# Performance work log

Measured on AMD Instinct MI355X. Metric: run time of the kernel, lower is better.

Reference implementation:

```python
import jax, jax.numpy as jnp
import numpy as np

N_HEAD = 16
N_EMBD = 64  # per-head dim in this module's convention
INNER = N_HEAD * N_EMBD  # 1024


def setup_inputs() -> dict:
    key = jax.random.key(0)
    ks = jax.random.split(key, 6)
    B, S = 4, 2048
    scale = 0.02
    return {
        "x": jax.random.normal(ks[0], (B, S, N_EMBD), dtype=jnp.float32),
        "Wq": jax.random.normal(ks[1], (N_EMBD, INNER), dtype=jnp.float32) * scale,
        "Wk": jax.random.normal(ks[2], (N_EMBD, INNER), dtype=jnp.float32) * scale,
        "Wv": jax.random.normal(ks[3], (N_EMBD, INNER), dtype=jnp.float32) * scale,
        "Wo": jax.random.normal(ks[4], (INNER, N_EMBD), dtype=jnp.float32) * scale,
        "bo": jax.random.normal(ks[5], (N_EMBD,), dtype=jnp.float32) * scale,
        "causal_mask": 1,
    }


def reference(x, Wq, Wk, Wv, Wo, bo, causal_mask):
    B, S, _ = x.shape
    # projections: [B,S,INNER] -> [B,H,S,D]
    def split_heads(t):
        return t.reshape(B, S, N_HEAD, N_EMBD).transpose(0, 2, 1, 3)
    q = split_heads(x @ Wq)
    k = split_heads(x @ Wk)
    v = split_heads(x @ Wv)
    # [B,H,S,S]
    scores = jnp.einsum("bhqd,bhkd->bhqk", q, k) / jnp.sqrt(jnp.float32(N_EMBD))
    if causal_mask:
        future = jnp.triu(jnp.ones((S, S), dtype=scores.dtype), k=1)
        scores = scores - 1e9 * future  # matches torch: subtract 1e9*mask
    attn = jax.nn.softmax(scores, axis=-1)
    out = jnp.einsum("bhqk,bhkd->bhqd", attn, v)
    out = out.transpose(0, 2, 1, 3).reshape(B, S, INNER)
    return out @ Wo + bo
```

## Files before the change

kernel.cpp:

```cpp
#include <hip/hip_runtime.h>
#include <hip/hip_bf16.h>

#define NHEAD 16
#define HDIM 64
#define DINNER 1024
#define NBATCH 4
#define SEQ 2048
#define NTOK (NBATCH*SEQ)

typedef __bf16 bf16;
typedef __bf16 bf16x4 __attribute__((ext_vector_type(4)));
typedef __bf16 bf16x8 __attribute__((ext_vector_type(8)));
typedef float f32x4 __attribute__((ext_vector_type(4)));

#define OFF_BO   8
#define OFF_XB   128
#define OFF_WQT  (OFF_XB + NTOK*HDIM)
#define OFF_WKT  (OFF_WQT + DINNER*HDIM)
#define OFF_WVT  (OFF_WKT + DINNER*HDIM)
#define OFF_WOT  (OFF_WVT + DINNER*HDIM)
#define OFF_Q    (OFF_WOT + DINNER*HDIM)
#define OFF_K    (OFF_Q + NTOK*DINNER)
#define OFF_VT   (OFF_K + NTOK*DINNER)
#define OFF_ATT  (OFF_VT + NTOK*DINNER)

#define SSCALE 0.18033688011112042f

static __device__ __forceinline__ bf16x8 ld8(const bf16* p) {
  return *reinterpret_cast<const bf16x8*>(p);
}

static __device__ __forceinline__ int detect_isbf(const void* x, int tid,
                                                  int* sflag) {
  if (tid < 64) {
    const unsigned short* xb = (const unsigned short*)x;
    bool ok = true;
#pragma unroll
    for (int i = 0; i < 8; i++) {
      unsigned e = (xb[tid * 8 + i] >> 7) & 0xFF;
      ok = ok && (e >= 64 && e <= 140);
    }
    unsigned long long mball = __ballot(ok);
    if (tid == 0) *sflag = (mball == ~0ull) ? 1 : 0;
  }
  __syncthreads();
  return *sflag;
}

__global__ __launch_bounds__(256) void prep_kernel(
    const void* __restrict__ x, const void* __restrict__ Wq,
    const void* __restrict__ Wk, const void* __restrict__ Wv,
    const void* __restrict__ Wo, const void* __restrict__ bo,
    bf16* __restrict__ ws) {
  __shared__ int sflag;
  int isbf = detect_isbf(x, threadIdx.x, &sflag);
  int z = blockIdx.y;
  int idx = blockIdx.x * 256 + threadIdx.x;
  if (z < 3) {
    const void* src = (z == 0) ? Wq : (z == 1) ? Wk : Wv;
    bf16* dst = ws + ((z == 0) ? OFF_WQT : (z == 1) ? OFF_WKT : OFF_WVT);
    int d = idx >> 10, n = idx & 1023;
    float v = isbf ? (float)((const bf16*)src)[idx] : ((const float*)src)[idx];
    if (z == 0) v *= SSCALE;
    dst[n * HDIM + d] = (bf16)v;
  } else if (z == 3) {
    int k = idx >> 6, n = idx & 63;
    float v = isbf ? (float)((const bf16*)Wo)[idx] : ((const float*)Wo)[idx];
    ws[OFF_WOT + n * DINNER + k] = (bf16)v;
  } else if (z == 4) {
    int i = idx * 8;
    bf16x8 v;
    if (isbf) {
      v = ld8((const bf16*)x + i);
    } else {
      f32x4 a = *reinterpret_cast<const f32x4*>((const float*)x + i);
      f32x4 b2 = *reinterpret_cast<const f32x4*>((const float*)x + i + 4);
#pragma unroll
      for (int j = 0; j < 4; j++) { v[j] = (bf16)a[j]; v[4 + j] = (bf16)b2[j]; }
    }
    *reinterpret_cast<bf16x8*>(&ws[OFF_XB + i]) = v;
  } else {
    if (idx < 64) ws[OFF_BO + idx] = isbf ? ((const bf16*)bo)[idx] : (bf16)((const float*)bo)[idx];
  }
}

__global__ __launch_bounds__(256) void qkv_kernel(bf16* __restrict__ ws) {
  __shared__ __align__(16) bf16 Vst[4][16 * 72];
  int tt = blockIdx.x, pz = blockIdx.z;
  int w = threadIdx.x >> 6;
  int nc = blockIdx.y * 4 + w;
  int lane = threadIdx.x & 63;
  int lq = lane & 15, quad = lane >> 4;
  const bf16* WT = ws + OFF_WQT + pz * (DINNER * HDIM);
  int n0 = nc * 64;
  bf16x8 w0[4], w1[4];
#pragma unroll
  for (int c = 0; c < 4; c++) {
    const bf16* wr = WT + (n0 + c * 16 + lq) * HDIM;
    w0[c] = ld8(wr + quad * 8);
    w1[c] = ld8(wr + 32 + quad * 8);
  }
  bf16* Qb = ws + OFF_Q;
  bf16* Kb = ws + OFF_K;
  bf16* VTb = ws + OFF_VT;
  bf16x8 ao0[4], ao1[4];
  if (pz == 2) {
    const bf16* WoT = ws + OFF_WOT;
#pragma unroll
    for (int c = 0; c < 4; c++) {
      const bf16* orow = WoT + (size_t)(c * 16 + lq) * DINNER + nc * 64;
      ao0[c] = ld8(orow + quad * 8);
      ao1[c] = ld8(orow + 32 + quad * 8);
    }
  }
#pragma unroll
  for (int mi = 0; mi < 4; mi++) {
    int t0 = tt * 64 + mi * 16;
    const bf16* xrow = ws + OFF_XB + (t0 + lq) * HDIM;
    bf16x8 x0 = ld8(xrow + quad * 8);
    bf16x8 x1 = ld8(xrow + 32 + quad * 8);
    int b = t0 >> 11, s0 = t0 & (SEQ - 1);
    if (pz < 2) {
#pragma unroll
      for (int c = 0; c < 4; c++) {
        f32x4 z = {0.f, 0.f, 0.f, 0.f};
        z = __builtin_amdgcn_mfma_f32_16x16x32_bf16(w0[c], x0, z, 0, 0, 0);
        z = __builtin_amdgcn_mfma_f32_16x16x32_bf16(w1[c], x1, z, 0, 0, 0);
        bf16x4 pk = {(bf16)z[0], (bf16)z[1], (bf16)z[2], (bf16)z[3]};
        bf16* P = (pz == 0) ? Qb : Kb;
        *reinterpret_cast<bf16x4*>(
            &P[((size_t)(b * NHEAD + nc) * SEQ + s0 + lq) * HDIM + c * 16 + quad * 4]) = pk;
      }
    } else {
#pragma unroll
      for (int c = 0; c < 4; c++) {
        f32x4 z = {0.f, 0.f, 0.f, 0.f};
        z = __builtin_amdgcn_mfma_f32_16x16x32_bf16(w0[c], x0, z, 0, 0, 0);
        z = __builtin_amdgcn_mfma_f32_16x16x32_bf16(w1[c], x1, z, 0, 0, 0);
        bf16x4 pk = {(bf16)z[0], (bf16)z[1], (bf16)z[2], (bf16)z[3]};
        *reinterpret_cast<bf16x4*>(&Vst[w][lq * 72 + c * 16 + quad * 4]) = pk;
      }
      bf16x8 bv0 = ld8(&Vst[w][lq * 72 + quad * 8]);
      bf16x8 bv1 = ld8(&Vst[w][lq * 72 + 32 + quad * 8]);
#pragma unroll
      for (int c = 0; c < 4; c++) {
        f32x4 z2 = {0.f, 0.f, 0.f, 0.f};
        z2 = __builtin_amdgcn_mfma_f32_16x16x32_bf16(ao0[c], bv0, z2, 0, 0, 0);
        z2 = __builtin_amdgcn_mfma_f32_16x16x32_bf16(ao1[c], bv1, z2, 0, 0, 0);
#pragma unroll
        for (int r = 0; r < 4; r++) {
          int d = c * 16 + quad * 4 + r;
          VTb[(((size_t)b * NHEAD + nc) * HDIM + d) * SEQ + s0 + lq] = (bf16)z2[r];
        }
      }
    }
  }
}

__global__ __launch_bounds__(256, 2) void flash_kernel(const int* __restrict__ cmask,
                                                       bf16* __restrict__ ws) {
  __shared__ __align__(16) bf16 Kl[2][64 * 64];
  __shared__ __align__(16) bf16 Vl[2][64 * 64];
  __shared__ __align__(16) bf16 Pl[4][16 * 64];
  const int qmap[16] = {15,13,11,9,0,2,4,6,14,12,10,8,1,3,5,7};
  int bid = blockIdx.x;
  int bh = (bid & 7) * 8 + ((bid >> 3) & 7);
  int qt = qmap[bid >> 6];
  int w = threadIdx.x >> 6;
  int lane = threadIdx.x & 63;
  int lq = lane & 15, quad = lane >> 4;
  int causal = cmask[0];
  const bf16* Q = ws + OFF_Q + (size_t)bh * SEQ * HDIM;
  const bf16* K = ws + OFF_K + (size_t)bh * SEQ * HDIM;
  const bf16* VT = ws + OFF_VT + (size_t)bh * HDIM * SEQ;
  int b = bh >> 4, h = bh & 15;
  bf16* ar = ws + OFF_ATT;
  int sr = threadIdx.x >> 2;
  int sg = (threadIdx.x & 3) * 16;
  int sc0 = (((threadIdx.x & 3) * 2) ^ (sr & 7)) << 3;
  int sc1 = (((threadIdx.x & 3) * 2 + 1) ^ (sr & 7)) << 3;
  int rq0 = (quad ^ (lq & 7)) << 3;
  int rq1 = ((4 + quad) ^ (lq & 7)) << 3;

  int qb = qt * 128;
  int qw = qb + w * 32;
  int T = (causal ? (qb + 128) : SEQ) / 64;

  bf16x8 bq[2][2];
#pragma unroll
  for (int m = 0; m < 2; m++) {
    const bf16* qrow = Q + (qw + m * 16 + lq) * HDIM;
    bq[m][0] = ld8(qrow + quad * 8);
    bq[m][1] = ld8(qrow + 32 + quad * 8);
  }
  f32x4 o[2][4];
  float lsum[2] = {0.f, 0.f};
#pragma unroll
  for (int m = 0; m < 2; m++)
#pragma unroll
    for (int c = 0; c < 4; c++) o[m][c] = (f32x4){0.f, 0.f, 0.f, 0.f};

  bf16x8 kst0 = ld8(K + sr * HDIM + sg);
  bf16x8 kst1 = ld8(K + sr * HDIM + sg + 8);
  bf16x8 vst0 = ld8(VT + sr * SEQ + sg);
  bf16x8 vst1 = ld8(VT + sr * SEQ + sg + 8);

  for (int ti = 0; ti < T; ti++) {
    int buf = ti & 1;
    int k0 = ti * 64;
    *reinterpret_cast<bf16x8*>(&Kl[buf][sr * 64 + sc0]) = kst0;
    *reinterpret_cast<bf16x8*>(&Kl[buf][sr * 64 + sc1]) = kst1;
    *reinterpret_cast<bf16x8*>(&Vl[buf][sr * 64 + sc0]) = vst0;
    *reinterpret_cast<bf16x8*>(&Vl[buf][sr * 64 + sc1]) = vst1;
    int kn = (ti + 1 < T) ? (k0 + 64) : k0;
    kst0 = ld8(K + (kn + sr) * HDIM + sg);
    kst1 = ld8(K + (kn + sr) * HDIM + sg + 8);
    vst0 = ld8(VT + sr * SEQ + kn + sg);
    vst1 = ld8(VT + sr * SEQ + kn + sg + 8);
    __syncthreads();
    f32x4 st[2][4];
#pragma unroll
    for (int t = 0; t < 4; t++) {
      bf16x8 a0 = ld8(&Kl[buf][(t * 16 + lq) * 64 + rq0]);
      bf16x8 a1 = ld8(&Kl[buf][(t * 16 + lq) * 64 + rq1]);
#pragma unroll
      for (int m = 0; m < 2; m++) {
        f32x4 z = {0.f, 0.f, 0.f, 0.f};
        z = __builtin_amdgcn_mfma_f32_16x16x32_bf16(a0, bq[m][0], z, 0, 0, 0);
        z = __builtin_amdgcn_mfma_f32_16x16x32_bf16(a1, bq[m][1], z, 0, 0, 0);
        st[m][t] = z;
      }
    }
    bool needmask = causal && (k0 + 63 > qw);
    bf16x8 bp[2][2];
#pragma unroll
    for (int m = 0; m < 2; m++) {
      if (needmask) {
        int qrel = qw + m * 16 + lq - k0 - quad * 4;
#pragma unroll
        for (int t = 0; t < 4; t++)
#pragma unroll
          for (int r = 0; r < 4; r++)
            if (t * 16 + r > qrel) st[m][t][r] = -200.0f;
      }
      float sum = 0.f;
#pragma unroll
      for (int t = 0; t < 4; t++) {
        float e0 = exp2f(st[m][t][0]);
        float e1 = exp2f(st[m][t][1]);
        float e2 = exp2f(st[m][t][2]);
        float e3 = exp2f(st[m][t][3]);
        sum += (e0 + e1) + (e2 + e3);
        bf16x4 pk = {(bf16)e0, (bf16)e1, (bf16)e2, (bf16)e3};
        int ch = ((t * 2 + (quad >> 1)) ^ (lq & 7)) << 3;
        *reinterpret_cast<bf16x4*>(&Pl[w][lq * 64 + ch + (quad & 1) * 4]) = pk;
      }
      lsum[m] += sum;
      bp[m][0] = ld8(&Pl[w][lq * 64 + rq0]);
      bp[m][1] = ld8(&Pl[w][lq * 64 + rq1]);
    }
#pragma unroll
    for (int c = 0; c < 4; c++) {
      bf16x8 av0 = ld8(&Vl[buf][(c * 16 + lq) * 64 + rq0]);
      bf16x8 av1 = ld8(&Vl[buf][(c * 16 + lq) * 64 + rq1]);
#pragma unroll
      for (int m = 0; m < 2; m++) {
        o[m][c] = __builtin_amdgcn_mfma_f32_16x16x32_bf16(av0, bp[m][0], o[m][c], 0, 0, 0);
        o[m][c] = __builtin_amdgcn_mfma_f32_16x16x32_bf16(av1, bp[m][1], o[m][c], 0, 0, 0);
      }
    }
  }
#pragma unroll
  for (int m = 0; m < 2; m++) {
    lsum[m] += __shfl_xor(lsum[m], 16);
    lsum[m] += __shfl_xor(lsum[m], 32);
    float inv = 1.0f / lsum[m];
    size_t rowoff = ((size_t)(b * SEQ + qw + m * 16 + lq)) * DINNER + h * HDIM;
#pragma unroll
    for (int c = 0; c < 4; c++) {
      bf16x4 ov = {(bf16)(o[m][c][0] * inv), (bf16)(o[m][c][1] * inv),
                   (bf16)(o[m][c][2] * inv), (bf16)(o[m][c][3] * inv)};
      *reinterpret_cast<bf16x4*>(&ar[rowoff + c * 16 + quad * 4]) = ov;
    }
  }
}

__global__ __launch_bounds__(256) void reduce_kernel(const bf16* __restrict__ ws,
                                                     const void* __restrict__ x,
                                                     void* __restrict__ outp) {
  __shared__ int sflag;
  int isbf = detect_isbf(x, threadIdx.x, &sflag);
  int idx = blockIdx.x * 256 + threadIdx.x;
  int t = idx >> 6, d = idx & 63;
  const bf16* ar = ws + OFF_ATT + (size_t)t * DINNER + d;
  float s = (float)ws[OFF_BO + d];
#pragma unroll
  for (int h = 0; h < 16; h++) s += (float)ar[h * 64];
  if (isbf) ((bf16*)outp)[idx] = (bf16)s;
  else      ((float*)outp)[idx] = s;
}

extern "C" void kernel_launch(void* const* d_in, const int* in_sizes, int n_in,
                              void* d_out, int out_size, void* d_ws, size_t ws_size,
                              hipStream_t stream) {
  const void* x  = d_in[0];
  const void* Wq = d_in[1];
  const void* Wk = d_in[2];
  const void* Wv = d_in[3];
  const void* Wo = d_in[4];
  const void* bo = d_in[5];
  const int* cm  = (const int*)d_in[6];
  bf16* ws = (bf16*)d_ws;

  hipLaunchKernelGGL(prep_kernel, dim3(256, 6), dim3(256), 0, stream,
                     x, Wq, Wk, Wv, Wo, bo, ws);
  hipLaunchKernelGGL(qkv_kernel, dim3(128, 4, 3), dim3(256), 0, stream, ws);
  hipLaunchKernelGGL(flash_kernel, dim3(1024), dim3(256), 0, stream, cm, ws);
  hipLaunchKernelGGL(reduce_kernel, dim3(2048), dim3(256), 0, stream, ws, x, d_out);
}
```

Before: 161.8 us.

## Split causal KV range across paired query tiles for balanced flash blocks

Each flash block now handles a complementary pair of query tiles (z and 15-z) and processes one half of their combined KV tile range. This gives every block an equal amount of causal work. Unnormalized partial outputs and row sums are written to two workspace copies, and the reduce kernel merges them and normalizes. The launch-bounds occupancy hint is raised to 4. The split doubles the attention-output write and read traffic, and storing unnormalized accumulators in bf16 may cost some precision.

```diff
diff --git a/kernel.cpp b/kernel.cpp
--- a/kernel.cpp
+++ b/kernel.cpp
@@ -23,6 +23,8 @@
 #define OFF_K    (OFF_Q + NTOK*DINNER)
 #define OFF_VT   (OFF_K + NTOK*DINNER)
 #define OFF_ATT  (OFF_VT + NTOK*DINNER)
+#define OFF_ATT2 (OFF_ATT + NTOK*DINNER)
+#define OFF_L    (OFF_ATT2 + NTOK*DINNER)
 
 #define SSCALE 0.18033688011112042f
 
@@ -157,15 +159,15 @@
   }
 }
 
-__global__ __launch_bounds__(256, 2) void flash_kernel(const int* __restrict__ cmask,
+__global__ __launch_bounds__(256, 4) void flash_kernel(const int* __restrict__ cmask,
                                                        bf16* __restrict__ ws) {
   __shared__ __align__(16) bf16 Kl[2][64 * 64];
   __shared__ __align__(16) bf16 Vl[2][64 * 64];
   __shared__ __align__(16) bf16 Pl[4][16 * 64];
-  const int qmap[16] = {15,13,11,9,0,2,4,6,14,12,10,8,1,3,5,7};
   int bid = blockIdx.x;
   int bh = (bid & 7) * 8 + ((bid >> 3) & 7);
-  int qt = qmap[bid >> 6];
+  int z = (bid >> 6) & 7;
+  int half = bid >> 9;
   int w = threadIdx.x >> 6;
   int lane = threadIdx.x & 63;
   int lq = lane & 15, quad = lane >> 4;
@@ -174,7 +176,8 @@
   const bf16* K = ws + OFF_K + (size_t)bh * SEQ * HDIM;
   const bf16* VT = ws + OFF_VT + (size_t)bh * HDIM * SEQ;
   int b = bh >> 4, h = bh & 15;
-  bf16* ar = ws + OFF_ATT;
+  bf16* ar = ws + OFF_ATT + (size_t)half * NTOK * DINNER;
+  float* Lp = reinterpret_cast<float*>(ws + OFF_L) + (size_t)half * NTOK * NHEAD;
   int sr = threadIdx.x >> 2;
   int sg = (threadIdx.x & 3) * 16;
   int sc0 = (((threadIdx.x & 3) * 2) ^ (sr & 7)) << 3;
@@ -182,105 +185,120 @@
   int rq0 = (quad ^ (lq & 7)) << 3;
   int rq1 = ((4 + quad) ^ (lq & 7)) << 3;
 
-  int qb = qt * 128;
-  int qw = qb + w * 32;
-  int T = (causal ? (qb + 128) : SEQ) / 64;
-
-  bf16x8 bq[2][2];
-#pragma unroll
-  for (int m = 0; m < 2; m++) {
-    const bf16* qrow = Q + (qw + m * 16 + lq) * HDIM;
-    bq[m][0] = ld8(qrow + quad * 8);
-    bq[m][1] = ld8(qrow + 32 + quad * 8);
-  }
-  f32x4 o[2][4];
-  float lsum[2] = {0.f, 0.f};
-#pragma unroll
-  for (int m = 0; m < 2; m++)
-#pragma unroll
-    for (int c = 0; c < 4; c++) o[m][c] = (f32x4){0.f, 0.f, 0.f, 0.f};
-
-  bf16x8 kst0 = ld8(K + sr * HDIM + sg);
-  bf16x8 kst1 = ld8(K + sr * HDIM + sg + 8);
-  bf16x8 vst0 = ld8(VT + sr * SEQ + sg);
-  bf16x8 vst1 = ld8(VT + sr * SEQ + sg + 8);
-
-  for (int ti = 0; ti < T; ti++) {
-    int buf = ti & 1;
-    int k0 = ti * 64;
-    *reinterpret_cast<bf16x8*>(&Kl[buf][sr * 64 + sc0]) = kst0;
-    *reinterpret_cast<bf16x8*>(&Kl[buf][sr * 64 + sc1]) = kst1;
-    *reinterpret_cast<bf16x8*>(&Vl[buf][sr * 64 + sc0]) = vst0;
-    *reinterpret_cast<bf16x8*>(&Vl[buf][sr * 64 + sc1]) = vst1;
-    int kn = (ti + 1 < T) ? (k0 + 64) : k0;
-    kst0 = ld8(K + (kn + sr) * HDIM + sg);
-    kst1 = ld8(K + (kn + sr) * HDIM + sg + 8);
-    vst0 = ld8(VT + sr * SEQ + kn + sg);
-    vst1 = ld8(VT + sr * SEQ + kn + sg + 8);
-    __syncthreads();
-    f32x4 st[2][4];
-#pragma unroll
-    for (int t = 0; t < 4; t++) {
-      bf16x8 a0 = ld8(&Kl[buf][(t * 16 + lq) * 64 + rq0]);
-      bf16x8 a1 = ld8(&Kl[buf][(t * 16 + lq) * 64 + rq1]);
-#pragma unroll
-      for (int m = 0; m < 2; m++) {
-        f32x4 z = {0.f, 0.f, 0.f, 0.f};
-        z = __builtin_amdgcn_mfma_f32_16x16x32_bf16(a0, bq[m][0], z, 0, 0, 0);
-        z = __builtin_amdgcn_mfma_f32_16x16x32_bf16(a1, bq[m][1], z, 0, 0, 0);
-        st[m][t] = z;
-      }
-    }
-    bool needmask = causal && (k0 + 63 > qw);
-    bf16x8 bp[2][2];
+  int Ta = causal ? (2 * z + 2) : 32;
+  int Tb = causal ? (32 - 2 * z) : 32;
+  int chunk = (Ta + Tb) >> 1;
+  int c0 = half * chunk, c1 = c0 + chunk;
+  int bufc = 0;
+
+  for (int seg = 0; seg < 2; ++seg) {
+    int qt = seg ? (15 - z) : z;
+    int Ts = seg ? Tb : Ta;
+    int base = seg ? Ta : 0;
+    int t0 = c0 - base; t0 = t0 < 0 ? 0 : (t0 > Ts ? Ts : t0);
+    int t1 = c1 - base; t1 = t1 < 0 ? 0 : (t1 > Ts ? Ts : t1);
+    int qb = qt * 128;
+    int qw = qb + w * 32;
+
+    bf16x8 bq[2][2];
 #pragma unroll
     for (int m = 0; m < 2; m++) {
-      if (needmask) {
-        int qrel = qw + m * 16 + lq - k0 - quad * 4;
-#pragma unroll
-        for (int t = 0; t < 4; t++)
-#pragma unroll
-          for (int r = 0; r < 4; r++)
-            if (t * 16 + r > qrel) st[m][t][r] = -200.0f;
-      }
-      float sum = 0.f;
-#pragma unroll
-      for (int t = 0; t < 4; t++) {
-        float e0 = exp2f(st[m][t][0]);
-        float e1 = exp2f(st[m][t][1]);
-        float e2 = exp2f(st[m][t][2]);
-        float e3 = exp2f(st[m][t][3]);
-        sum += (e0 + e1) + (e2 + e3);
-        bf16x4 pk = {(bf16)e0, (bf16)e1, (bf16)e2, (bf16)e3};
-        int ch = ((t * 2 + (quad >> 1)) ^ (lq & 7)) << 3;
-        *reinterpret_cast<bf16x4*>(&Pl[w][lq * 64 + ch + (quad & 1) * 4]) = pk;
-      }
-      lsum[m] += sum;
-      bp[m][0] = ld8(&Pl[w][lq * 64 + rq0]);
-      bp[m][1] = ld8(&Pl[w][lq * 64 + rq1]);
-    }
-#pragma unroll
-    for (int c = 0; c < 4; c++) {
-      bf16x8 av0 = ld8(&Vl[buf][(c * 16 + lq) * 64 + rq0]);
-      bf16x8 av1 = ld8(&Vl[buf][(c * 16 + lq) * 64 + rq1]);
-#pragma unroll
-      for (int m = 0; m < 2; m++) {
-        o[m][c] = __builtin_amdgcn_mfma_f32_16x16x32_bf16(av0, bp[m][0], o[m][c], 0, 0, 0);
-        o[m][c] = __builtin_amdgcn_mfma_f32_16x16x32_bf16(av1, bp[m][1], o[m][c], 0, 0, 0);
-      }
-    }
-  }
-#pragma unroll
-  for (int m = 0; m < 2; m++) {
-    lsum[m] += __shfl_xor(lsum[m], 16);
-    lsum[m] += __shfl_xor(lsum[m], 32);
-    float inv = 1.0f / lsum[m];
-    size_t rowoff = ((size_t)(b * SEQ + qw + m * 16 + lq)) * DINNER + h * HDIM;
-#pragma unroll
-    for (int c = 0; c < 4; c++) {
-      bf16x4 ov = {(bf16)(o[m][c][0] * inv), (bf16)(o[m][c][1] * inv),
-                   (bf16)(o[m][c][2] * inv), (bf16)(o[m][c][3] * inv)};
-      *reinterpret_cast<bf16x4*>(&ar[rowoff + c * 16 + quad * 4]) = ov;
+      const bf16* qrow = Q + (qw + m * 16 + lq) * HDIM;
+      bq[m][0] = ld8(qrow + quad * 8);
+      bq[m][1] = ld8(qrow + 32 + quad * 8);
+    }
+    f32x4 o[2][4];
+    float lsum[2] = {0.f, 0.f};
+#pragma unroll
+    for (int m = 0; m < 2; m++)
+#pragma unroll
+      for (int c = 0; c < 4; c++) o[m][c] = (f32x4){0.f, 0.f, 0.f, 0.f};
+
+    if (t0 < t1) {
+      bf16x8 kst0 = ld8(K + (size_t)(t0 * 64 + sr) * HDIM + sg);
+      bf16x8 kst1 = ld8(K + (size_t)(t0 * 64 + sr) * HDIM + sg + 8);
+      bf16x8 vst0 = ld8(VT + (size_t)sr * SEQ + t0 * 64 + sg);
+      bf16x8 vst1 = ld8(VT + (size_t)sr * SEQ + t0 * 64 + sg + 8);
+
+      for (int ti = t0; ti < t1; ++ti, ++bufc) {
+        int buf = bufc & 1;
+        int k0 = ti * 64;
+        *reinterpret_cast<bf16x8*>(&Kl[buf][sr * 64 + sc0]) = kst0;
+        *reinterpret_cast<bf16x8*>(&Kl[buf][sr * 64 + sc1]) = kst1;
+        *reinterpret_cast<bf16x8*>(&Vl[buf][sr * 64 + sc0]) = vst0;
+        *reinterpret_cast<bf16x8*>(&Vl[buf][sr * 64 + sc1]) = vst1;
+        int kn = (ti + 1 < t1) ? (k0 + 64) : k0;
+        kst0 = ld8(K + (size_t)(kn + sr) * HDIM + sg);
+        kst1 = ld8(K + (size_t)(kn + sr) * HDIM + sg + 8);
+        vst0 = ld8(VT + (size_t)sr * SEQ + kn + sg);
+        vst1 = ld8(VT + (size_t)sr * SEQ + kn + sg + 8);
+        __syncthreads();
+        f32x4 st[2][4];
+#pragma unroll
+        for (int t = 0; t < 4; t++) {
+          bf16x8 a0 = ld8(&Kl[buf][(t * 16 + lq) * 64 + rq0]);
+          bf16x8 a1 = ld8(&Kl[buf][(t * 16 + lq) * 64 + rq1]);
+#pragma unroll
+          for (int m = 0; m < 2; m++) {
+            f32x4 zz = {0.f, 0.f, 0.f, 0.f};
+            zz = __builtin_amdgcn_mfma_f32_16x16x32_bf16(a0, bq[m][0], zz, 0, 0, 0);
+            zz = __builtin_amdgcn_mfma_f32_16x16x32_bf16(a1, bq[m][1], zz, 0, 0, 0);
+            st[m][t] = zz;
+          }
+        }
+        bool needmask = causal && (k0 + 63 > qw);
+        bf16x8 bp[2][2];
+#pragma unroll
+        for (int m = 0; m < 2; m++) {
+          if (needmask) {
+            int qrel = qw + m * 16 + lq - k0 - quad * 4;
+#pragma unroll
+            for (int t = 0; t < 4; t++)
+#pragma unroll
+              for (int r = 0; r < 4; r++)
+                if (t * 16 + r > qrel) st[m][t][r] = -200.0f;
+          }
+          float sum = 0.f;
+#pragma unroll
+          for (int t = 0; t < 4; t++) {
+            float e0 = exp2f(st[m][t][0]);
+            float e1 = exp2f(st[m][t][1]);
+            float e2 = exp2f(st[m][t][2]);
+            float e3 = exp2f(st[m][t][3]);
+            sum += (e0 + e1) + (e2 + e3);
+            bf16x4 pk = {(bf16)e0, (bf16)e1, (bf16)e2, (bf16)e3};
+            int ch = ((t * 2 + (quad >> 1)) ^ (lq & 7)) << 3;
+            *reinterpret_cast<bf16x4*>(&Pl[w][lq * 64 + ch + (quad & 1) * 4]) = pk;
+          }
+          lsum[m] += sum;
+          bp[m][0] = ld8(&Pl[w][lq * 64 + rq0]);
+          bp[m][1] = ld8(&Pl[w][lq * 64 + rq1]);
+        }
+#pragma unroll
+        for (int c = 0; c < 4; c++) {
+          bf16x8 av0 = ld8(&Vl[buf][(c * 16 + lq) * 64 + rq0]);
+          bf16x8 av1 = ld8(&Vl[buf][(c * 16 + lq) * 64 + rq1]);
+#pragma unroll
+          for (int m = 0; m < 2; m++) {
+            o[m][c] = __builtin_amdgcn_mfma_f32_16x16x32_bf16(av0, bp[m][0], o[m][c], 0, 0, 0);
+            o[m][c] = __builtin_amdgcn_mfma_f32_16x16x32_bf16(av1, bp[m][1], o[m][c], 0, 0, 0);
+          }
+        }
+      }
+    }
+#pragma unroll
+    for (int m = 0; m < 2; m++) {
+      lsum[m] += __shfl_xor(lsum[m], 16);
+      lsum[m] += __shfl_xor(lsum[m], 32);
+      size_t row = (size_t)(b * SEQ + qw + m * 16 + lq);
+      if (quad == 0) Lp[row * NHEAD + h] = lsum[m];
+      size_t rowoff = row * DINNER + (size_t)h * HDIM;
+#pragma unroll
+      for (int c = 0; c < 4; c++) {
+        bf16x4 ov = {(bf16)o[m][c][0], (bf16)o[m][c][1],
+                     (bf16)o[m][c][2], (bf16)o[m][c][3]};
+        *reinterpret_cast<bf16x4*>(&ar[rowoff + c * 16 + quad * 4]) = ov;
+      }
     }
   }
 }
@@ -292,10 +310,16 @@
   int isbf = detect_isbf(x, threadIdx.x, &sflag);
   int idx = blockIdx.x * 256 + threadIdx.x;
   int t = idx >> 6, d = idx & 63;
-  const bf16* ar = ws + OFF_ATT + (size_t)t * DINNER + d;
+  const bf16* a0 = ws + OFF_ATT + (size_t)t * DINNER + d;
+  const bf16* a1 = a0 + (size_t)NTOK * DINNER;
+  const float* l0 = reinterpret_cast<const float*>(ws + OFF_L) + (size_t)t * NHEAD;
+  const float* l1 = l0 + (size_t)NTOK * NHEAD;
   float s = (float)ws[OFF_BO + d];
 #pragma unroll
-  for (int h = 0; h < 16; h++) s += (float)ar[h * 64];
+  for (int h = 0; h < 16; h++) {
+    float inv = 1.0f / (l0[h] + l1[h]);
+    s += ((float)a0[h * 64] + (float)a1[h * 64]) * inv;
+  }
   if (isbf) ((bf16*)outp)[idx] = (bf16)s;
   else      ((float*)outp)[idx] = s;
 }
```

Result: slower. 172.9 us (+6.9%).

## Fuse weight/input prep into QKV kernel and vectorize V-transpose stores

Applied to the files above, without the earlier changes.

Removes the separate prep kernel: the QKV kernel now reads raw fp32 or bf16 x and weights directly, converting them and transposing the weights through per-wave shared memory. This saves one launch and a round trip of converted data through the workspace. It also swaps the MFMA operand order for the Wo·V product so V^T is written with 4-wide vector stores instead of scalar scattered stores. The cost is that every block redoes the weight conversion and transpose in LDS, which is redundant work across the 128 token tiles.

```diff
diff --git a/kernel.cpp b/kernel.cpp
--- a/kernel.cpp
+++ b/kernel.cpp
@@ -9,116 +9,151 @@
 #define NTOK (NBATCH*SEQ)
 
 typedef __bf16 bf16;
+typedef __bf16 bf16x2 __attribute__((ext_vector_type(2)));
 typedef __bf16 bf16x4 __attribute__((ext_vector_type(4)));
 typedef __bf16 bf16x8 __attribute__((ext_vector_type(8)));
 typedef float f32x4 __attribute__((ext_vector_type(4)));
 
-#define OFF_BO   8
-#define OFF_XB   128
-#define OFF_WQT  (OFF_XB + NTOK*HDIM)
-#define OFF_WKT  (OFF_WQT + DINNER*HDIM)
-#define OFF_WVT  (OFF_WKT + DINNER*HDIM)
-#define OFF_WOT  (OFF_WVT + DINNER*HDIM)
-#define OFF_Q    (OFF_WOT + DINNER*HDIM)
-#define OFF_K    (OFF_Q + NTOK*DINNER)
-#define OFF_VT   (OFF_K + NTOK*DINNER)
-#define OFF_ATT  (OFF_VT + NTOK*DINNER)
+#define OFF_Q    0
+#define OFF_K    ((size_t)NTOK*DINNER)
+#define OFF_VT   ((size_t)2*NTOK*DINNER)
+#define OFF_ATT  ((size_t)3*NTOK*DINNER)
 
 #define SSCALE 0.18033688011112042f
 
 static __device__ __forceinline__ bf16x8 ld8(const bf16* p) {
   return *reinterpret_cast<const bf16x8*>(p);
+}
+
+static __device__ __forceinline__ int detect_isbf_wave(const void* x, int lane) {
+  const unsigned short* xb = (const unsigned short*)x;
+  bool ok = true;
+#pragma unroll
+  for (int i = 0; i < 8; i++) {
+    unsigned e = (xb[lane * 8 + i] >> 7) & 0xFF;
+    ok = ok && (e >= 64 && e <= 140);
+  }
+  return (__ballot(ok) == ~0ull) ? 1 : 0;
 }
 
 static __device__ __forceinline__ int detect_isbf(const void* x, int tid,
                                                   int* sflag) {
   if (tid < 64) {
-    const unsigned short* xb = (const unsigned short*)x;
-    bool ok = true;
-#pragma unroll
-    for (int i = 0; i < 8; i++) {
-      unsigned e = (xb[tid * 8 + i] >> 7) & 0xFF;
-      ok = ok && (e >= 64 && e <= 140);
-    }
-    unsigned long long mball = __ballot(ok);
-    if (tid == 0) *sflag = (mball == ~0ull) ? 1 : 0;
+    int r = detect_isbf_wave(x, tid & 63);
+    if (tid == 0) *sflag = r;
   }
   __syncthreads();
   return *sflag;
 }
 
-__global__ __launch_bounds__(256) void prep_kernel(
+__global__ __launch_bounds__(256) void qkv_kernel(
     const void* __restrict__ x, const void* __restrict__ Wq,
     const void* __restrict__ Wk, const void* __restrict__ Wv,
-    const void* __restrict__ Wo, const void* __restrict__ bo,
-    bf16* __restrict__ ws) {
-  __shared__ int sflag;
-  int isbf = detect_isbf(x, threadIdx.x, &sflag);
-  int z = blockIdx.y;
-  int idx = blockIdx.x * 256 + threadIdx.x;
-  if (z < 3) {
-    const void* src = (z == 0) ? Wq : (z == 1) ? Wk : Wv;
-    bf16* dst = ws + ((z == 0) ? OFF_WQT : (z == 1) ? OFF_WKT : OFF_WVT);
-    int d = idx >> 10, n = idx & 1023;
-    float v = isbf ? (float)((const bf16*)src)[idx] : ((const float*)src)[idx];
-    if (z == 0) v *= SSCALE;
-    dst[n * HDIM + d] = (bf16)v;
-  } else if (z == 3) {
-    int k = idx >> 6, n = idx & 63;
-    float v = isbf ? (float)((const bf16*)Wo)[idx] : ((const float*)Wo)[idx];
-    ws[OFF_WOT + n * DINNER + k] = (bf16)v;
-  } else if (z == 4) {
-    int i = idx * 8;
+    const void* __restrict__ Wo, bf16* __restrict__ ws) {
+  __shared__ __align__(16) bf16 Wt[4][64 * 66];
+  int tt = blockIdx.x, pz = blockIdx.z;
+  int w = threadIdx.x >> 6;
+  int lane = threadIdx.x & 63;
+  int lq = lane & 15, quad = lane >> 4;
+  int isbf = detect_isbf_wave(x, lane);
+  int nc = blockIdx.y * 4 + w;
+  int n0 = nc * 64;
+  bf16* T = Wt[w];
+  int drow = lane >> 3, chunk = lane & 7;
+
+  const void* Wsrc = (pz == 0) ? Wq : (pz == 1) ? Wk : Wv;
+#pragma unroll
+  for (int p = 0; p < 8; p++) {
+    int d = p * 8 + drow;
     bf16x8 v;
     if (isbf) {
-      v = ld8((const bf16*)x + i);
+      bf16x8 raw = ld8((const bf16*)Wsrc + (size_t)d * DINNER + n0 + chunk * 8);
+      if (pz == 0) {
+#pragma unroll
+        for (int j = 0; j < 8; j++) v[j] = (bf16)((float)raw[j] * SSCALE);
+      } else {
+        v = raw;
+      }
     } else {
-      f32x4 a = *reinterpret_cast<const f32x4*>((const float*)x + i);
-      f32x4 b2 = *reinterpret_cast<const f32x4*>((const float*)x + i + 4);
+      const float* s = (const float*)Wsrc + (size_t)d * DINNER + n0 + chunk * 8;
+      f32x4 a = *reinterpret_cast<const f32x4*>(s);
+      f32x4 b2 = *reinterpret_cast<const f32x4*>(s + 4);
+      if (pz == 0) {
+#pragma unroll
+        for (int j = 0; j < 4; j++) { a[j] *= SSCALE; b2[j] *= SSCALE; }
+      }
 #pragma unroll
       for (int j = 0; j < 4; j++) { v[j] = (bf16)a[j]; v[4 + j] = (bf16)b2[j]; }
     }
-    *reinterpret_cast<bf16x8*>(&ws[OFF_XB + i]) = v;
-  } else {
-    if (idx < 64) ws[OFF_BO + idx] = isbf ? ((const bf16*)bo)[idx] : (bf16)((const float*)bo)[idx];
-  }
-}
-
-__global__ __launch_bounds__(256) void qkv_kernel(bf16* __restrict__ ws) {
-  __shared__ __align__(16) bf16 Vst[4][16 * 72];
-  int tt = blockIdx.x, pz = blockIdx.z;
-  int w = threadIdx.x >> 6;
-  int nc = blockIdx.y * 4 + w;
-  int lane = threadIdx.x & 63;
-  int lq = lane & 15, quad = lane >> 4;
-  const bf16* WT = ws + OFF_WQT + pz * (DINNER * HDIM);
-  int n0 = nc * 64;
+#pragma unroll
+    for (int i = 0; i < 4; i++) {
+      bf16x2 t2; t2[0] = v[2 * i]; t2[1] = v[2 * i + 1];
+      *reinterpret_cast<bf16x2*>(&T[d * 66 + chunk * 8 + 2 * i]) = t2;
+    }
+  }
   bf16x8 w0[4], w1[4];
 #pragma unroll
   for (int c = 0; c < 4; c++) {
-    const bf16* wr = WT + (n0 + c * 16 + lq) * HDIM;
-    w0[c] = ld8(wr + quad * 8);
-    w1[c] = ld8(wr + 32 + quad * 8);
+#pragma unroll
+    for (int j = 0; j < 8; j++) {
+      w0[c][j] = T[(quad * 8 + j) * 66 + c * 16 + lq];
+      w1[c][j] = T[(32 + quad * 8 + j) * 66 + c * 16 + lq];
+    }
+  }
+  bf16x8 ao0[4], ao1[4];
+  if (pz == 2) {
+#pragma unroll
+    for (int p = 0; p < 8; p++) {
+      int kl = p * 8 + drow;
+      bf16x8 v;
+      if (isbf) {
+        v = ld8((const bf16*)Wo + (size_t)(n0 + kl) * HDIM + chunk * 8);
+      } else {
+        const float* s = (const float*)Wo + (size_t)(n0 + kl) * HDIM + chunk * 8;
+        f32x4 a = *reinterpret_cast<const f32x4*>(s);
+        f32x4 b2 = *reinterpret_cast<const f32x4*>(s + 4);
+#pragma unroll
+        for (int j = 0; j < 4; j++) { v[j] = (bf16)a[j]; v[4 + j] = (bf16)b2[j]; }
+      }
+#pragma unroll
+      for (int i = 0; i < 4; i++) {
+        bf16x2 t2; t2[0] = v[2 * i]; t2[1] = v[2 * i + 1];
+        *reinterpret_cast<bf16x2*>(&T[kl * 66 + chunk * 8 + 2 * i]) = t2;
+      }
+    }
+#pragma unroll
+    for (int c = 0; c < 4; c++) {
+#pragma unroll
+      for (int j = 0; j < 8; j++) {
+        ao0[c][j] = T[(quad * 8 + j) * 66 + c * 16 + lq];
+        ao1[c][j] = T[(32 + quad * 8 + j) * 66 + c * 16 + lq];
+      }
+    }
   }
   bf16* Qb = ws + OFF_Q;
   bf16* Kb = ws + OFF_K;
   bf16* VTb = ws + OFF_VT;
-  bf16x8 ao0[4], ao1[4];
-  if (pz == 2) {
-    const bf16* WoT = ws + OFF_WOT;
-#pragma unroll
-    for (int c = 0; c < 4; c++) {
-      const bf16* orow = WoT + (size_t)(c * 16 + lq) * DINNER + nc * 64;
-      ao0[c] = ld8(orow + quad * 8);
-      ao1[c] = ld8(orow + 32 + quad * 8);
-    }
-  }
+  bf16* Vst = T;
 #pragma unroll
   for (int mi = 0; mi < 4; mi++) {
     int t0 = tt * 64 + mi * 16;
-    const bf16* xrow = ws + OFF_XB + (t0 + lq) * HDIM;
-    bf16x8 x0 = ld8(xrow + quad * 8);
-    bf16x8 x1 = ld8(xrow + 32 + quad * 8);
+    bf16x8 x0, x1;
+    if (isbf) {
+      const bf16* xrow = (const bf16*)x + (size_t)(t0 + lq) * HDIM;
+      x0 = ld8(xrow + quad * 8);
+      x1 = ld8(xrow + 32 + quad * 8);
+    } else {
+      const float* xrow = (const float*)x + (size_t)(t0 + lq) * HDIM;
+      f32x4 a0 = *reinterpret_cast<const f32x4*>(xrow + quad * 8);
+      f32x4 a1 = *reinterpret_cast<const f32x4*>(xrow + quad * 8 + 4);
+      f32x4 b0 = *reinterpret_cast<const f32x4*>(xrow + 32 + quad * 8);
+      f32x4 b1 = *reinterpret_cast<const f32x4*>(xrow + 32 + quad * 8 + 4);
+#pragma unroll
+      for (int j = 0; j < 4; j++) {
+        x0[j] = (bf16)a0[j]; x0[4 + j] = (bf16)a1[j];
+        x1[j] = (bf16)b0[j]; x1[4 + j] = (bf16)b1[j];
+      }
+    }
     int b = t0 >> 11, s0 = t0 & (SEQ - 1);
     if (pz < 2) {
 #pragma unroll
@@ -138,20 +173,18 @@
         z = __builtin_amdgcn_mfma_f32_16x16x32_bf16(w0[c], x0, z, 0, 0, 0);
         z = __builtin_amdgcn_mfma_f32_16x16x32_bf16(w1[c], x1, z, 0, 0, 0);
         bf16x4 pk = {(bf16)z[0], (bf16)z[1], (bf16)z[2], (bf16)z[3]};
-        *reinterpret_cast<bf16x4*>(&Vst[w][lq * 72 + c * 16 + quad * 4]) = pk;
-      }
-      bf16x8 bv0 = ld8(&Vst[w][lq * 72 + quad * 8]);
-      bf16x8 bv1 = ld8(&Vst[w][lq * 72 + 32 + quad * 8]);
+        *reinterpret_cast<bf16x4*>(&Vst[lq * 72 + c * 16 + quad * 4]) = pk;
+      }
+      bf16x8 bv0 = ld8(&Vst[lq * 72 + quad * 8]);
+      bf16x8 bv1 = ld8(&Vst[lq * 72 + 32 + quad * 8]);
 #pragma unroll
       for (int c = 0; c < 4; c++) {
         f32x4 z2 = {0.f, 0.f, 0.f, 0.f};
-        z2 = __builtin_amdgcn_mfma_f32_16x16x32_bf16(ao0[c], bv0, z2, 0, 0, 0);
-        z2 = __builtin_amdgcn_mfma_f32_16x16x32_bf16(ao1[c], bv1, z2, 0, 0, 0);
-#pragma unroll
-        for (int r = 0; r < 4; r++) {
-          int d = c * 16 + quad * 4 + r;
-          VTb[(((size_t)b * NHEAD + nc) * HDIM + d) * SEQ + s0 + lq] = (bf16)z2[r];
-        }
+        z2 = __builtin_amdgcn_mfma_f32_16x16x32_bf16(bv0, ao0[c], z2, 0, 0, 0);
+        z2 = __builtin_amdgcn_mfma_f32_16x16x32_bf16(bv1, ao1[c], z2, 0, 0, 0);
+        bf16x4 pk = {(bf16)z2[0], (bf16)z2[1], (bf16)z2[2], (bf16)z2[3]};
+        *reinterpret_cast<bf16x4*>(
+            &VTb[(((size_t)b * NHEAD + nc) * HDIM + c * 16 + lq) * SEQ + s0 + quad * 4]) = pk;
       }
     }
   }
@@ -287,13 +320,14 @@
 
 __global__ __launch_bounds__(256) void reduce_kernel(const bf16* __restrict__ ws,
                                                      const void* __restrict__ x,
+                                                     const void* __restrict__ bo,
                                                      void* __restrict__ outp) {
   __shared__ int sflag;
   int isbf = detect_isbf(x, threadIdx.x, &sflag);
   int idx = blockIdx.x * 256 + threadIdx.x;
   int t = idx >> 6, d = idx & 63;
   const bf16* ar = ws + OFF_ATT + (size_t)t * DINNER + d;
-  float s = (float)ws[OFF_BO + d];
+  float s = isbf ? (float)((const bf16*)bo)[d] : ((const float*)bo)[d];
 #pragma unroll
   for (int h = 0; h < 16; h++) s += (float)ar[h * 64];
   if (isbf) ((bf16*)outp)[idx] = (bf16)s;
@@ -312,9 +346,8 @@
   const int* cm  = (const int*)d_in[6];
   bf16* ws = (bf16*)d_ws;
 
-  hipLaunchKernelGGL(prep_kernel, dim3(256, 6), dim3(256), 0, stream,
-                     x, Wq, Wk, Wv, Wo, bo, ws);
-  hipLaunchKernelGGL(qkv_kernel, dim3(128, 4, 3), dim3(256), 0, stream, ws);
+  hipLaunchKernelGGL(qkv_kernel, dim3(128, 4, 3), dim3(256), 0, stream,
+                     x, Wq, Wk, Wv, Wo, ws);
   hipLaunchKernelGGL(flash_kernel, dim3(1024), dim3(256), 0, stream, cm, ws);
-  hipLaunchKernelGGL(reduce_kernel, dim3(2048), dim3(256), 0, stream, ws, x, d_out);
-}
+  hipLaunchKernelGGL(reduce_kernel, dim3(2048), dim3(256), 0, stream, ws, x, bo, d_out);
+}
```

After: 166.3 us. 2.8% more time.
